# Kernel tuning notes

Hardware: AMD Instinct MI355X
Metric: run time of the kernel (lower is better)

The kernel has to match this reference:

```python
import jax, jax.numpy as jnp
import numpy as np

B, N, D, M, C = 4, 256, 128, 128, 128


def _lin_init(key, din, dout):
    # torch nn.Linear default: U(-1/sqrt(din), 1/sqrt(din)) for weight and bias
    bound = 1.0 / np.sqrt(din)
    kw, kb = jax.random.split(key)
    W = jax.random.uniform(kw, (din, dout), jnp.float32, -bound, bound)
    b = jax.random.uniform(kb, (dout,), jnp.float32, -bound, bound)
    return W, b


def setup_inputs() -> dict:
    key = jax.random.key(0)
    k_h, k_adj, k1, k2, k3, k4 = jax.random.split(key, 6)
    h = jax.random.normal(k_h, (B, N, D), jnp.float32)
    adj = jax.random.uniform(k_adj, (B, N, N), jnp.float32)
    # msg MLP: Linear(2D -> M), SiLU, Linear(M -> M). Split first weight into
    # the h_i block (W1a) and h_j block (W1b) of the concatenated input.
    W1, b1 = _lin_init(k1, 2 * D, M)
    W1a, W1b = W1[:D], W1[D:]
    W2, b2 = _lin_init(k2, M, M)
    # to_c MLP: Linear(M -> M), SiLU, Linear(M -> C)
    Wc1, bc1 = _lin_init(k3, M, M)
    Wc2, bc2 = _lin_init(k4, M, C)
    return {"h": h, "adj": adj, "W1a": W1a, "W1b": W1b, "b1": b1,
            "W2": W2, "b2": b2, "Wc1": Wc1, "bc1": bc1, "Wc2": Wc2, "bc2": bc2}


def reference(h, adj, W1a, W1b, b1, W2, b2, Wc1, bc1, Wc2, bc2):
    n = h.shape[1]
    # First msg Linear on cat([h_i, h_j]) == h_i @ W1a + h_j @ W1b + b1.
    # Precompute per-node projections once instead of the (B,N,N,2D) pair tensor.
    pi = jnp.einsum('bnd,dm->bnm', h, W1a)           # (B,N,M) for destination i
    pj = jnp.einsum('bnd,dm->bnm', h, W1b)           # (B,N,M) for source j
    pre = pi[:, :, None, :] + pj[:, None, :, :] + b1  # (B,N,N,M)
    m = jnp.einsum('bijm,mk->bijk', jax.nn.silu(pre), W2) + b2  # (B,N,N,M)
    # zero self-messages (diagonal ignored), then weight by adjacency
    mask = (1.0 - jnp.eye(n, dtype=h.dtype))[None, :, :, None]
    m = m * mask * adj[..., None]
    # mean aggregation over source nodes j with clamped degree
    denom = jnp.clip(jnp.sum(adj, axis=-1, keepdims=True), 1.0)  # (B,N,1)
    m_agg = jnp.sum(m, axis=2) / denom                           # (B,N,M)
    c = jnp.einsum('bnm,mc->bnc', jax.nn.silu(jnp.einsum('bnm,mk->bnk', m_agg, Wc1) + bc1), Wc2) + bc2
    return c
```

## Files before the change

kernel.cpp:

```cpp
#include <hip/hip_runtime.h>
#include <math.h>

#define BB 4
#define NN 256
#define DD 128
#define MM 128
#define CC 128
#define ROWS (BB * NN)
#define RPB 4
#define NBLK (ROWS / RPB)
#define TPB 512

#define L2E 1.44269504088896340736f

static __device__ __forceinline__ float fast_exp2(float x) {
#if __has_builtin(__builtin_amdgcn_exp2f)
    return __builtin_amdgcn_exp2f(x);
#else
    return __exp2f(x);
#endif
}

static __device__ __forceinline__ float fast_rcp(float x) {
#if __has_builtin(__builtin_amdgcn_rcpf)
    return __builtin_amdgcn_rcpf(x);
#else
    return 1.0f / x;
#endif
}

static __device__ __forceinline__ float silu_f(float x) {
    float e = fast_exp2(-L2E * x);
    return x * fast_rcp(1.0f + e);
}

#if __has_builtin(__builtin_amdgcn_global_load_lds)
#define HAS_GLDS 1
#define GLDS(gp, lp)                                                        \
    __builtin_amdgcn_global_load_lds(                                       \
        (const __attribute__((address_space(1))) void*)(gp),                \
        (__attribute__((address_space(3))) void*)(lp), 16, 0, 0)
#else
#define HAS_GLDS 0
#endif

template <int ITERS>
static __device__ __forceinline__ void stage_lin(float* lds, const float* g,
                                                 int t) {
#if HAS_GLDS
    const int wv = t >> 6, lane = t & 63;
    #pragma unroll
    for (int i = 0; i < ITERS; ++i) {
        const int c = i * 8 + wv;
        GLDS(g + (size_t)c * 256 + lane * 4, lds + c * 256);
    }
#else
    #pragma unroll
    for (int i = 0; i < ITERS; ++i)
        ((float4*)lds)[i * TPB + t] = ((const float4*)g)[i * TPB + t];
#endif
}

__global__ __launch_bounds__(TPB) void k_proj(const float* __restrict__ h,
                                              const float* __restrict__ W1a,
                                              const float* __restrict__ W1b,
                                              const float* __restrict__ b1,
                                              float* __restrict__ pibias,
                                              float* __restrict__ pj) {
    __shared__ float sW[128 * 256];
    __shared__ float sH[RPB * DD];

    const int t = threadIdx.x;
    const int m = t & 127;
    const int q = t >> 7;
    const int row0 = blockIdx.x * RPB;

    sH[t] = h[(size_t)row0 * DD + t];

#if HAS_GLDS
    {
        const int wv = t >> 6, lane = t & 63;
        #pragma unroll
        for (int i = 0; i < 16; ++i) {
            const int r = i * 8 + wv;
            const float* g = (lane < 32)
                                 ? (W1a + (size_t)r * 128 + lane * 4)
                                 : (W1b + (size_t)r * 128 + (lane - 32) * 4);
            GLDS(g, &sW[r * 256]);
        }
    }
#else
    #pragma unroll
    for (int i = 0; i < 16; ++i) {
        const int f = i * TPB + t;
        const int r = f >> 6;
        const int c4 = f & 63;
        const float4 v = (c4 < 32)
                             ? ((const float4*)(W1a + (size_t)r * 128))[c4]
                             : ((const float4*)(W1b + (size_t)r * 128))[c4 - 32];
        ((float4*)sW)[f] = v;
    }
#endif

    const float bias = b1[m];
    __syncthreads();

    float accA = 0.0f, accB = 0.0f;
    const float* sHq = &sH[q * DD];
    #pragma unroll 8
    for (int d = 0; d < 128; d += 2) {
        const float2 hv = *(const float2*)&sHq[d];
        accA = fmaf(hv.x, sW[d * 256 + m], accA);
        accB = fmaf(hv.x, sW[d * 256 + 128 + m], accB);
        accA = fmaf(hv.y, sW[(d + 1) * 256 + m], accA);
        accB = fmaf(hv.y, sW[(d + 1) * 256 + 128 + m], accB);
    }

    pibias[(size_t)row0 * MM + t] = accA + bias;
    pj[(size_t)row0 * MM + t]     = accB;
}

__global__ __launch_bounds__(TPB) void k_msgout(const float* __restrict__ adj,
                                                const float* __restrict__ pibias,
                                                const float* __restrict__ pj,
                                                const float* __restrict__ W2,
                                                const float* __restrict__ b2,
                                                const float* __restrict__ Wc1,
                                                const float* __restrict__ bc1,
                                                const float* __restrict__ Wc2,
                                                const float* __restrict__ bc2,
                                                float* __restrict__ out) {
    __shared__ float sPJ[256 * MM];
    __shared__ float sAdj[RPB][NN];
    __shared__ float sS[RPB * MM];
    __shared__ float sB[RPB * MM];
    __shared__ float sWr0[8];
    __shared__ float sWr1[8];

    const int t = threadIdx.x;
    const int blk = blockIdx.x;
    const int b = blk >> 6;
    const int i0 = (blk & 63) * RPB;
    const int row0 = b * NN + i0;

    const int m = t & 127;
    const int q = t >> 7;
    const int w = t >> 6;

    const float* __restrict__ pjB = pj + (size_t)b * NN * MM;
    stage_lin<16>(sPJ, pjB, t);

    const float pim  = pibias[(size_t)(row0 + q) * MM + m];
    const float b2k  = b2[m];
    const float bc1k = bc1[m];
    const float bc2k = bc2[m];

    const float* arow = adj + (size_t)row0 * NN;
    const float a0v = arow[t];
    const float a1v = arow[t + TPB];
    float* sA = &sAdj[0][0];
    sA[t] = a0v;
    sA[t + TPB] = a1v;

    float v0 = a0v, v1 = a1v;
    #pragma unroll
    for (int off = 32; off > 0; off >>= 1) {
        v0 += __shfl_xor(v0, off, 64);
        v1 += __shfl_xor(v1, off, 64);
    }
    if ((t & 63) == 0) { sWr0[w] = v0; sWr1[w] = v1; }

    __syncthreads();

    float A;
    {
        const int base = (q & 1) * 4;
        A = (q < 2) ? (sWr0[base] + sWr0[base + 1] + sWr0[base + 2] + sWr0[base + 3])
                    : (sWr1[base] + sWr1[base + 1] + sWr1[base + 2] + sWr1[base + 3]);
    }
    const float aii = sAdj[q][i0 + q];
    const float inv = 1.0f / fmaxf(A, 1.0f);
    const float bet = (A - aii) * inv;
    const float npim = -L2E * pim;

    float acc = -aii * silu_f(pim + sPJ[(i0 + q) * MM + m]);

    #pragma unroll 8
    for (int j = 0; j < 128; j += 2) {
        const float p0 = sPJ[j * MM + m];
        const float p1 = sPJ[(j + 1) * MM + m];
        const float2 wv = *(const float2*)&sAdj[q][j];
        const float x0 = pim + p0, x1 = pim + p1;
        const float e0 = fast_exp2(fmaf(-L2E, p0, npim));
        const float e1 = fast_exp2(fmaf(-L2E, p1, npim));
        const float d0 = 1.0f + e0, d1 = 1.0f + e1;
        const float rp = fast_rcp(d0 * d1);
        acc = fmaf(wv.x * x0, rp * d1, acc);
        acc = fmaf(wv.y * x1, rp * d0, acc);
    }

    __syncthreads();
    stage_lin<8>(sPJ, W2, t);

    #pragma unroll 8
    for (int j = 128; j < 256; j += 2) {
        const float p0 = sPJ[j * MM + m];
        const float p1 = sPJ[(j + 1) * MM + m];
        const float2 wv = *(const float2*)&sAdj[q][j];
        const float x0 = pim + p0, x1 = pim + p1;
        const float e0 = fast_exp2(fmaf(-L2E, p0, npim));
        const float e1 = fast_exp2(fmaf(-L2E, p1, npim));
        const float d0 = 1.0f + e0, d1 = 1.0f + e1;
        const float rp = fast_rcp(d0 * d1);
        acc = fmaf(wv.x * x0, rp * d1, acc);
        acc = fmaf(wv.y * x1, rp * d0, acc);
    }
    sS[q * MM + m] = acc * inv;

    __syncthreads();
    stage_lin<8>(sPJ + 16384, Wc1, t);

    float acc2 = bet * b2k;
    {
        const float* sSr = &sS[q * MM];
        #pragma unroll 8
        for (int d = 0; d < 128; d += 2) {
            const float2 sv = *(const float2*)&sSr[d];
            acc2 = fmaf(sv.x, sPJ[d * MM + m], acc2);
            acc2 = fmaf(sv.y, sPJ[(d + 1) * MM + m], acc2);
        }
    }
    sB[q * MM + m] = acc2;

    __syncthreads();
    stage_lin<8>(sPJ, Wc2, t);

    acc2 = bc1k;
    {
        const float* sBr = &sB[q * MM];
        const float* sW1 = sPJ + 16384;
        #pragma unroll 8
        for (int d = 0; d < 128; d += 2) {
            const float2 sv = *(const float2*)&sBr[d];
            acc2 = fmaf(sv.x, sW1[d * MM + m], acc2);
            acc2 = fmaf(sv.y, sW1[(d + 1) * MM + m], acc2);
        }
    }
    sS[q * MM + m] = silu_f(acc2);

    __syncthreads();

    acc2 = bc2k;
    {
        const float* sSr = &sS[q * MM];
        #pragma unroll 8
        for (int d = 0; d < 128; d += 2) {
            const float2 sv = *(const float2*)&sSr[d];
            acc2 = fmaf(sv.x, sPJ[d * MM + m], acc2);
            acc2 = fmaf(sv.y, sPJ[(d + 1) * MM + m], acc2);
        }
    }
    out[(size_t)row0 * CC + t] = acc2;
}

extern "C" void kernel_launch(void* const* d_in, const int* in_sizes, int n_in,
                              void* d_out, int out_size, void* d_ws, size_t ws_size,
                              hipStream_t stream) {
    const float* h   = (const float*)d_in[0];
    const float* adj = (const float*)d_in[1];
    const float* W1a = (const float*)d_in[2];
    const float* W1b = (const float*)d_in[3];
    const float* b1  = (const float*)d_in[4];
    const float* W2  = (const float*)d_in[5];
    const float* b2  = (const float*)d_in[6];
    const float* Wc1 = (const float*)d_in[7];
    const float* bc1 = (const float*)d_in[8];
    const float* Wc2 = (const float*)d_in[9];
    const float* bc2 = (const float*)d_in[10];
    float* out = (float*)d_out;

    float* ws = (float*)d_ws;
    float* pibias = ws;
    float* pj     = ws + (size_t)ROWS * MM;

    k_proj<<<NBLK, TPB, 0, stream>>>(h, W1a, W1b, b1, pibias, pj);
    k_msgout<<<NBLK, TPB, 0, stream>>>(adj, pibias, pj, W2, b2, Wc1, bc1,
                                       Wc2, bc2, out);
}
```

Measured before the change: 97.81 us.

## Transpose pj and MLP weights into XOR-swizzled layout for float4 LDS reads

k_proj now writes pj transposed (m-major, j inner) with an XOR swizzle and also transposes W2, Wc1 and Wc2 into a swizzled workspace layout. k_msgout then reads four consecutive j or d values per thread as one float4 LDS load instead of separate scalar loads. Adjacency values are read straight from global memory through a wave-uniform row pointer rather than staged in LDS. The aim is fewer LDS instructions and bank conflicts in the inner loops. The cost is scattered global writes in k_proj and extra work for the first 12 blocks.

```diff
diff --git a/kernel.cpp b/kernel.cpp
--- a/kernel.cpp
+++ b/kernel.cpp
@@ -13,6 +13,13 @@
 
 #define L2E 1.44269504088896340736f
 
+#define WS_PIB   0
+#define WS_PJLO  131072
+#define WS_PJHI  196608
+#define WS_W2T   262144
+#define WS_WC1T  278528
+#define WS_WC2T  294912
+
 static __device__ __forceinline__ float fast_exp2(float x) {
 #if __has_builtin(__builtin_amdgcn_exp2f)
     return __builtin_amdgcn_exp2f(x);
@@ -65,9 +72,11 @@
                                               const float* __restrict__ W1a,
                                               const float* __restrict__ W1b,
                                               const float* __restrict__ b1,
-                                              float* __restrict__ pibias,
-                                              float* __restrict__ pj) {
-    __shared__ float sW[128 * 256];
+                                              const float* __restrict__ W2,
+                                              const float* __restrict__ Wc1,
+                                              const float* __restrict__ Wc2,
+                                              float* __restrict__ ws) {
+    __shared__ __align__(16) float sW[128 * 256];
     __shared__ float sH[RPB * DD];
 
     const int t = threadIdx.x;
@@ -116,26 +125,45 @@
         accB = fmaf(hv.y, sW[(d + 1) * 256 + 128 + m], accB);
     }
 
-    pibias[(size_t)row0 * MM + t] = accA + bias;
-    pj[(size_t)row0 * MM + t]     = accB;
+    ws[WS_PIB + (size_t)row0 * MM + t] = accA + bias;
+
+    {
+        const int b    = row0 >> 8;
+        const int jloc = (row0 & 255) + q;
+        const int half = jloc >> 7;
+        const int jj   = jloc & 127;
+        const int c16  = jj >> 2;
+        const int off  = (half ? WS_PJHI : WS_PJLO) + b * 16384 + m * 128 +
+                         (((c16 ^ (m & 7)) << 2) | (jj & 3));
+        ws[off] = accB;
+    }
+
+    if (blockIdx.x < 12) {
+        const int blk = blockIdx.x;
+        const float* Wsrc = (blk < 4) ? W2 : (blk < 8) ? Wc1 : Wc2;
+        float* Wdst = ws + ((blk < 4) ? WS_W2T : (blk < 8) ? WS_WC1T : WS_WC2T);
+        const int d0 = (blk & 3) * 32;
+        const int k = m;
+        #pragma unroll
+        for (int i = 0; i < 8; ++i) {
+            const int d = d0 + (q << 3) + i;
+            const float v = Wsrc[(size_t)d * 128 + k];
+            Wdst[k * 128 + ((((d >> 2) ^ (k & 7)) << 2) | (d & 3))] = v;
+        }
+    }
 }
 
 __global__ __launch_bounds__(TPB) void k_msgout(const float* __restrict__ adj,
-                                                const float* __restrict__ pibias,
-                                                const float* __restrict__ pj,
-                                                const float* __restrict__ W2,
                                                 const float* __restrict__ b2,
-                                                const float* __restrict__ Wc1,
                                                 const float* __restrict__ bc1,
-                                                const float* __restrict__ Wc2,
                                                 const float* __restrict__ bc2,
+                                                const float* __restrict__ ws,
                                                 float* __restrict__ out) {
-    __shared__ float sPJ[256 * MM];
-    __shared__ float sAdj[RPB][NN];
-    __shared__ float sS[RPB * MM];
-    __shared__ float sB[RPB * MM];
-    __shared__ float sWr0[8];
-    __shared__ float sWr1[8];
+    __shared__ __align__(16) float sLo[16384];
+    __shared__ __align__(16) float sHi[16384];
+    __shared__ __align__(16) float sS[RPB * MM];
+    __shared__ __align__(16) float sB[RPB * MM];
+    __shared__ float sWr0[8], sWr1[8];
 
     const int t = threadIdx.x;
     const int blk = blockIdx.x;
@@ -146,11 +174,12 @@
     const int m = t & 127;
     const int q = t >> 7;
     const int w = t >> 6;
-
-    const float* __restrict__ pjB = pj + (size_t)b * NN * MM;
-    stage_lin<16>(sPJ, pjB, t);
-
-    const float pim  = pibias[(size_t)(row0 + q) * MM + m];
+    const int swz = m & 7;
+
+    stage_lin<8>(sLo, ws + WS_PJLO + b * 16384, t);
+    stage_lin<8>(sHi, ws + WS_PJHI + b * 16384, t);
+
+    const float pim  = ws[WS_PIB + (size_t)row0 * MM + t];
     const float b2k  = b2[m];
     const float bc1k = bc1[m];
     const float bc2k = bc2[m];
@@ -158,10 +187,6 @@
     const float* arow = adj + (size_t)row0 * NN;
     const float a0v = arow[t];
     const float a1v = arow[t + TPB];
-    float* sA = &sAdj[0][0];
-    sA[t] = a0v;
-    sA[t + TPB] = a1v;
-
     float v0 = a0v, v1 = a1v;
     #pragma unroll
     for (int off = 32; off > 0; off >>= 1) {
@@ -170,6 +195,9 @@
     }
     if ((t & 63) == 0) { sWr0[w] = v0; sWr1[w] = v1; }
 
+    const int srow = __builtin_amdgcn_readfirstlane(row0 + q);
+    const float* __restrict__ adjr = adj + (size_t)srow * NN;
+
     __syncthreads();
 
     float A;
@@ -178,86 +206,113 @@
         A = (q < 2) ? (sWr0[base] + sWr0[base + 1] + sWr0[base + 2] + sWr0[base + 3])
                     : (sWr1[base] + sWr1[base + 1] + sWr1[base + 2] + sWr1[base + 3]);
     }
-    const float aii = sAdj[q][i0 + q];
+    const float aii = adjr[srow & 255];
     const float inv = 1.0f / fmaxf(A, 1.0f);
     const float bet = (A - aii) * inv;
     const float npim = -L2E * pim;
 
-    float acc = -aii * silu_f(pim + sPJ[(i0 + q) * MM + m]);
-
+    float acc;
+    {
+        const int iloc = i0 + q;
+        const int jj = iloc & 127;
+        const float* base = (iloc < 128) ? sLo : sHi;
+        const float pjd = base[m * 128 + ((((jj >> 2) ^ swz) << 2) | (jj & 3))];
+        acc = -aii * silu_f(pim + pjd);
+    }
+
+    const float* rowLo = sLo + m * 128;
     #pragma unroll 8
-    for (int j = 0; j < 128; j += 2) {
-        const float p0 = sPJ[j * MM + m];
-        const float p1 = sPJ[(j + 1) * MM + m];
-        const float2 wv = *(const float2*)&sAdj[q][j];
-        const float x0 = pim + p0, x1 = pim + p1;
-        const float e0 = fast_exp2(fmaf(-L2E, p0, npim));
-        const float e1 = fast_exp2(fmaf(-L2E, p1, npim));
+    for (int j4 = 0; j4 < 32; ++j4) {
+        const float4 pv = *(const float4*)(rowLo + ((j4 ^ swz) << 2));
+        const float4 av = *(const float4*)(adjr + (j4 << 2));
+        const float x0 = pim + pv.x, x1 = pim + pv.y;
+        const float x2 = pim + pv.z, x3 = pim + pv.w;
+        const float e0 = fast_exp2(fmaf(-L2E, pv.x, npim));
+        const float e1 = fast_exp2(fmaf(-L2E, pv.y, npim));
+        const float e2 = fast_exp2(fmaf(-L2E, pv.z, npim));
+        const float e3 = fast_exp2(fmaf(-L2E, pv.w, npim));
         const float d0 = 1.0f + e0, d1 = 1.0f + e1;
-        const float rp = fast_rcp(d0 * d1);
-        acc = fmaf(wv.x * x0, rp * d1, acc);
-        acc = fmaf(wv.y * x1, rp * d0, acc);
-    }
-
-    __syncthreads();
-    stage_lin<8>(sPJ, W2, t);
-
+        const float d2 = 1.0f + e2, d3 = 1.0f + e3;
+        const float r01 = fast_rcp(d0 * d1), r23 = fast_rcp(d2 * d3);
+        acc = fmaf(av.x * x0, r01 * d1, acc);
+        acc = fmaf(av.y * x1, r01 * d0, acc);
+        acc = fmaf(av.z * x2, r23 * d3, acc);
+        acc = fmaf(av.w * x3, r23 * d2, acc);
+    }
+
+    __syncthreads();
+    stage_lin<8>(sLo, ws + WS_W2T, t);
+
+    const float* rowHi = sHi + m * 128;
     #pragma unroll 8
-    for (int j = 128; j < 256; j += 2) {
-        const float p0 = sPJ[j * MM + m];
-        const float p1 = sPJ[(j + 1) * MM + m];
-        const float2 wv = *(const float2*)&sAdj[q][j];
-        const float x0 = pim + p0, x1 = pim + p1;
-        const float e0 = fast_exp2(fmaf(-L2E, p0, npim));
-        const float e1 = fast_exp2(fmaf(-L2E, p1, npim));
+    for (int j4 = 0; j4 < 32; ++j4) {
+        const float4 pv = *(const float4*)(rowHi + ((j4 ^ swz) << 2));
+        const float4 av = *(const float4*)(adjr + 128 + (j4 << 2));
+        const float x0 = pim + pv.x, x1 = pim + pv.y;
+        const float x2 = pim + pv.z, x3 = pim + pv.w;
+        const float e0 = fast_exp2(fmaf(-L2E, pv.x, npim));
+        const float e1 = fast_exp2(fmaf(-L2E, pv.y, npim));
+        const float e2 = fast_exp2(fmaf(-L2E, pv.z, npim));
+        const float e3 = fast_exp2(fmaf(-L2E, pv.w, npim));
         const float d0 = 1.0f + e0, d1 = 1.0f + e1;
-        const float rp = fast_rcp(d0 * d1);
-        acc = fmaf(wv.x * x0, rp * d1, acc);
-        acc = fmaf(wv.y * x1, rp * d0, acc);
-    }
-    sS[q * MM + m] = acc * inv;
-
-    __syncthreads();
-    stage_lin<8>(sPJ + 16384, Wc1, t);
+        const float d2 = 1.0f + e2, d3 = 1.0f + e3;
+        const float r01 = fast_rcp(d0 * d1), r23 = fast_rcp(d2 * d3);
+        acc = fmaf(av.x * x0, r01 * d1, acc);
+        acc = fmaf(av.y * x1, r01 * d0, acc);
+        acc = fmaf(av.z * x2, r23 * d3, acc);
+        acc = fmaf(av.w * x3, r23 * d2, acc);
+    }
+    sS[(q << 7) + m] = acc * inv;
+
+    __syncthreads();
+    stage_lin<8>(sHi, ws + WS_WC1T, t);
 
     float acc2 = bet * b2k;
     {
-        const float* sSr = &sS[q * MM];
+        const float* rw = sLo + m * 128;
         #pragma unroll 8
-        for (int d = 0; d < 128; d += 2) {
-            const float2 sv = *(const float2*)&sSr[d];
-            acc2 = fmaf(sv.x, sPJ[d * MM + m], acc2);
-            acc2 = fmaf(sv.y, sPJ[(d + 1) * MM + m], acc2);
-        }
-    }
-    sB[q * MM + m] = acc2;
-
-    __syncthreads();
-    stage_lin<8>(sPJ, Wc2, t);
+        for (int d4 = 0; d4 < 32; ++d4) {
+            const float4 wv4 = *(const float4*)(rw + ((d4 ^ swz) << 2));
+            const float4 sv4 = *(const float4*)(&sS[(q << 7) + (d4 << 2)]);
+            acc2 = fmaf(sv4.x, wv4.x, acc2);
+            acc2 = fmaf(sv4.y, wv4.y, acc2);
+            acc2 = fmaf(sv4.z, wv4.z, acc2);
+            acc2 = fmaf(sv4.w, wv4.w, acc2);
+        }
+    }
+    sB[(q << 7) + m] = acc2;
+
+    __syncthreads();
+    stage_lin<8>(sLo, ws + WS_WC2T, t);
 
     acc2 = bc1k;
     {
-        const float* sBr = &sB[q * MM];
-        const float* sW1 = sPJ + 16384;
+        const float* rw = sHi + m * 128;
         #pragma unroll 8
-        for (int d = 0; d < 128; d += 2) {
-            const float2 sv = *(const float2*)&sBr[d];
-            acc2 = fmaf(sv.x, sW1[d * MM + m], acc2);
-            acc2 = fmaf(sv.y, sW1[(d + 1) * MM + m], acc2);
-        }
-    }
-    sS[q * MM + m] = silu_f(acc2);
+        for (int d4 = 0; d4 < 32; ++d4) {
+            const float4 wv4 = *(const float4*)(rw + ((d4 ^ swz) << 2));
+            const float4 sv4 = *(const float4*)(&sB[(q << 7) + (d4 << 2)]);
+            acc2 = fmaf(sv4.x, wv4.x, acc2);
+            acc2 = fmaf(sv4.y, wv4.y, acc2);
+            acc2 = fmaf(sv4.z, wv4.z, acc2);
+            acc2 = fmaf(sv4.w, wv4.w, acc2);
+        }
+    }
+    sS[(q << 7) + m] = silu_f(acc2);
 
     __syncthreads();
 
     acc2 = bc2k;
     {
-        const float* sSr = &sS[q * MM];
+        const float* rw = sLo + m * 128;
         #pragma unroll 8
-        for (int d = 0; d < 128; d += 2) {
-            const float2 sv = *(const float2*)&sSr[d];
-            acc2 = fmaf(sv.x, sPJ[d * MM + m], acc2);
-            acc2 = fmaf(sv.y, sPJ[(d + 1) * MM + m], acc2);
+        for (int d4 = 0; d4 < 32; ++d4) {
+            const float4 wv4 = *(const float4*)(rw + ((d4 ^ swz) << 2));
+            const float4 sv4 = *(const float4*)(&sS[(q << 7) + (d4 << 2)]);
+            acc2 = fmaf(sv4.x, wv4.x, acc2);
+            acc2 = fmaf(sv4.y, wv4.y, acc2);
+            acc2 = fmaf(sv4.z, wv4.z, acc2);
+            acc2 = fmaf(sv4.w, wv4.w, acc2);
         }
     }
     out[(size_t)row0 * CC + t] = acc2;
@@ -278,12 +333,8 @@
     const float* Wc2 = (const float*)d_in[9];
     const float* bc2 = (const float*)d_in[10];
     float* out = (float*)d_out;
-
-    float* ws = (float*)d_ws;
-    float* pibias = ws;
-    float* pj     = ws + (size_t)ROWS * MM;
-
-    k_proj<<<NBLK, TPB, 0, stream>>>(h, W1a, W1b, b1, pibias, pj);
-    k_msgout<<<NBLK, TPB, 0, stream>>>(adj, pibias, pj, W2, b2, Wc1, bc1,
-                                       Wc2, bc2, out);
-}
+    float* ws  = (float*)d_ws;
+
+    k_proj<<<NBLK, TPB, 0, stream>>>(h, W1a, W1b, b1, W2, Wc1, Wc2, ws);
+    k_msgout<<<NBLK, TPB, 0, stream>>>(adj, b2, bc1, bc2, ws, out);
+}
```

Measured after the change: 97.65 us. No clear change (-0.2%).
